# Kernel tuning notes

Hardware: AMD Instinct MI355X
Metric: run time of the kernel (lower is better)

Reference implementation:

```python
import jax, jax.numpy as jnp
import numpy as np

B, S, D, H = 128, 2048, 512, 512


def setup_inputs() -> dict:
    key = jax.random.key(0)
    ks = jax.random.split(key, 8)
    inputs = jax.random.normal(ks[0], (B, D), dtype=jnp.float32)
    contexts = jax.random.normal(ks[1], (B, S, D), dtype=jnp.float32)
    mask = jax.random.randint(ks[2], (B, S), 0, 2).astype(bool)  # True = masked out
    W_in = jax.random.normal(ks[3], (H, D), dtype=jnp.float32) * (1.0 / np.sqrt(D))
    b_in = jnp.zeros((H,), dtype=jnp.float32)
    W_ctx = jax.random.normal(ks[4], (H, D), dtype=jnp.float32) * (1.0 / np.sqrt(D))  # Conv1d k=1 weight
    b_ctx = jnp.zeros((H,), dtype=jnp.float32)
    V = jax.random.normal(ks[5], (H,), dtype=jnp.float32) * (1.0 / np.sqrt(H))
    return {"inputs": inputs, "contexts": contexts, "mask": mask,
            "W_in": W_in, "b_in": b_in, "W_ctx": W_ctx, "b_ctx": b_ctx, "V": V}


def reference(inputs, contexts, mask, W_in, b_in, W_ctx, b_ctx, V):
    # query projection (nn.Linear): [B, H]
    q = inputs @ W_in.T + b_in
    # context projection (Conv1d kernel=1 over permuted [B, D, S]): [B, H, S]
    ctx = jnp.einsum('hd,bsd->bhs', W_ctx, contexts) + b_ctx[None, :, None]
    # additive (Bahdanau) score: V . tanh(q + ctx) over H -> [B, S]
    att = jnp.einsum('h,bhs->bs', V, jnp.tanh(q[:, :, None] + ctx))
    att = jnp.where(mask, -jnp.inf, att)
    score = jax.nn.softmax(att, axis=1)  # nn.Softmax() on 2D -> dim=1 (S)
    # weighted sum of projected contexts: [B, H]
    hidden = jnp.einsum('bhs,bs->bh', ctx, score)
    return hidden, score
```

## Files before the change

kernel.cpp:

```cpp
#include <hip/hip_runtime.h>
#include <hip/hip_bf16.h>
#include <math.h>


#define B_N 128
#define S_N 2048
#define D_N 512
#define H_N 512

typedef __attribute__((ext_vector_type(8))) short bf16x8;
typedef __attribute__((ext_vector_type(4))) float f32x4;

__device__ __forceinline__ unsigned short f2bf(float x) {
  union { float f; unsigned int u; } v; v.f = x;
  unsigned int r = v.u + 0x7fffu + ((v.u >> 16) & 1u);
  return (unsigned short)(r >> 16);
}

__device__ __forceinline__ float tanh_fast(float x) {
  float ax = fabsf(x);
  float e = __expf(2.0f * ax);
  float t = 1.0f - 2.0f / (e + 1.0f);
  return copysignf(t, x);
}

__global__ void detect_mask_kernel(const unsigned int* __restrict__ mask,
                                   int* __restrict__ flag) {
  int tid = threadIdx.x;
  unsigned int bad = 0;
  for (int i = tid; i < 256; i += 64) bad |= (mask[i] > 1u) ? 1u : 0u;
  unsigned long long b = __ballot(bad != 0);
  if (tid == 0) *flag = (b == 0ull) ? 1 : 0;
}

__global__ __launch_bounds__(256) void packw_kernel(const float* __restrict__ Wc,
                                                    unsigned short* __restrict__ wpack) {
  int idx = blockIdx.x * 256 + threadIdx.x;
  int h = idx >> 9;
  int kg = idx & 511;
  int t = kg >> 6, kk = kg & 63;
  int byte = t * 65536 + h * 128 + ((kk * 2) ^ ((h & 7) << 4));
  *(unsigned short*)((char*)wpack + byte) = f2bf(Wc[idx]);
}

__global__ __launch_bounds__(256) void qproj_kernel(const float* __restrict__ inp,
    const float* __restrict__ Win, const float* __restrict__ bin,
    const float* __restrict__ bctx, float* __restrict__ qpb) {
  int b = blockIdx.x, tid = threadIdx.x;
  __shared__ float xin[D_N];
  xin[tid] = inp[b * D_N + tid];
  xin[tid + 256] = inp[b * D_N + tid + 256];
  __syncthreads();
  #pragma unroll
  for (int hh = 0; hh < 2; ++hh) {
    int h = tid + hh * 256;
    const float4* wrow = (const float4*)(Win + (size_t)h * D_N);
    float s = 0.f;
    #pragma unroll 4
    for (int i = 0; i < 128; ++i) {
      float4 w = wrow[i];
      s += w.x * xin[i*4] + w.y * xin[i*4+1] + w.z * xin[i*4+2] + w.w * xin[i*4+3];
    }
    qpb[b * H_N + h] = s + bin[h] + bctx[h];
  }
}

__global__ __launch_bounds__(512, 2) void att_kernel(
    const float* __restrict__ ctxs, const void* __restrict__ mask,
    const int* __restrict__ mflag,
    const unsigned short* __restrict__ wpack, const float* __restrict__ qpb,
    const float* __restrict__ Vp, float* __restrict__ att_out) {
  __shared__ char lds[16384 + 65536];
  char* sA = lds;
  char* sB = lds + 16384;
  float* att_red = (float*)lds;

  const int tid  = threadIdx.x;
  const int wid  = tid >> 6;
  const int lane = tid & 63;
  const int ln15 = lane & 15;
  const int lk   = lane >> 4;
  const int wr   = wid >> 2;
  const int wc   = wid & 3;

  const int bx = blockIdx.x;
  const int b  = bx >> 4;
  const int s0 = (bx & 15) * 128;

  f32x4 acc[4][8];
  #pragma unroll
  for (int mi = 0; mi < 4; ++mi)
    #pragma unroll
    for (int ni = 0; ni < 8; ++ni)
      acc[mi][ni] = (f32x4){0.f, 0.f, 0.f, 0.f};

  const float* actx = ctxs + ((size_t)b * S_N + s0) * D_N;

  for (int t = 0; t < 8; ++t) {
    const int k0 = t * 64;
    __syncthreads();
    #pragma unroll
    for (int i = 0; i < 4; ++i) {
      int p = i * 512 + tid;
      int r = p >> 4;
      int c = (p & 15) * 4;
      float4 v = *(const float4*)(actx + (size_t)r * D_N + k0 + c);
      unsigned int lo = (unsigned)f2bf(v.x) | ((unsigned)f2bf(v.y) << 16);
      unsigned int hi = (unsigned)f2bf(v.z) | ((unsigned)f2bf(v.w) << 16);
      int byte = r * 128 + ((c * 2) ^ ((r & 7) << 4));
      *(uint2*)(sA + byte) = make_uint2(lo, hi);
    }
    {
      const char* wsrc = (const char*)wpack + t * 65536;
      #pragma unroll
      for (int i = 0; i < 8; ++i) {
        int ci = wid * 8 + i;
        const char* g = wsrc + ci * 1024 + lane * 16;
        char* l = sB + ci * 1024 + lane * 16;
        __builtin_amdgcn_global_load_lds(
            (const __attribute__((address_space(1))) unsigned int*)g,
            (__attribute__((address_space(3))) unsigned int*)l, 16, 0, 0);
      }
    }
    __syncthreads();
    #pragma unroll
    for (int kk = 0; kk < 64; kk += 32) {
      const int kb2 = (kk + lk * 8) * 2;
      bf16x8 af[4];
      #pragma unroll
      for (int mi = 0; mi < 4; ++mi) {
        int r = wr * 64 + mi * 16 + ln15;
        af[mi] = *(const bf16x8*)(sA + r * 128 + (kb2 ^ ((r & 7) << 4)));
      }
      #pragma unroll
      for (int ni = 0; ni < 8; ++ni) {
        int h = wc * 128 + ni * 16 + ln15;
        bf16x8 bfr = *(const bf16x8*)(sB + h * 128 + (kb2 ^ ((h & 7) << 4)));
        #pragma unroll
        for (int mi = 0; mi < 4; ++mi)
          acc[mi][ni] = __builtin_amdgcn_mfma_f32_16x16x32_bf16(af[mi], bfr, acc[mi][ni], 0, 0, 0);
      }
    }
  }

  float qv[8], vv[8];
  #pragma unroll
  for (int ni = 0; ni < 8; ++ni) {
    int h = wc * 128 + ni * 16 + ln15;
    qv[ni] = qpb[b * H_N + h];
    vv[ni] = Vp[h];
  }
  float part[4][4];
  #pragma unroll
  for (int mi = 0; mi < 4; ++mi)
    #pragma unroll
    for (int j = 0; j < 4; ++j) {
      float s = 0.f;
      #pragma unroll
      for (int ni = 0; ni < 8; ++ni)
        s += vv[ni] * tanh_fast(qv[ni] + acc[mi][ni][j]);
      part[mi][j] = s;
    }
  #pragma unroll
  for (int mi = 0; mi < 4; ++mi)
    #pragma unroll
    for (int j = 0; j < 4; ++j) {
      float p = part[mi][j];
      p += __shfl_xor(p, 1, 64);
      p += __shfl_xor(p, 2, 64);
      p += __shfl_xor(p, 4, 64);
      p += __shfl_xor(p, 8, 64);
      part[mi][j] = p;
    }
  __syncthreads();
  if (ln15 == 0) {
    #pragma unroll
    for (int mi = 0; mi < 4; ++mi)
      #pragma unroll
      for (int j = 0; j < 4; ++j)
        att_red[wid * 64 + mi * 16 + lk * 4 + j] = part[mi][j];
  }
  __syncthreads();
  if (tid < 128) {
    int s = tid;
    int wrr = s >> 6, sl = s & 63;
    float a = att_red[(wrr * 4 + 0) * 64 + sl] + att_red[(wrr * 4 + 1) * 64 + sl]
            + att_red[(wrr * 4 + 2) * 64 + sl] + att_red[(wrr * 4 + 3) * 64 + sl];
    size_t idx = (size_t)b * S_N + s0 + s;
    int mk = (*mflag) ? ((const int*)mask)[idx]
                      : (int)((const unsigned char*)mask)[idx];
    att_out[idx] = mk ? -INFINITY : a;
  }
}

__global__ __launch_bounds__(256) void softmax_kernel(float* __restrict__ score) {
  int b = blockIdx.x, tid = threadIdx.x;
  float* row = score + (size_t)b * S_N;
  float v[8];
  float m = -INFINITY;
  #pragma unroll
  for (int i = 0; i < 8; ++i) { v[i] = row[tid + i * 256]; m = fmaxf(m, v[i]); }
  #pragma unroll
  for (int d = 1; d < 64; d <<= 1) m = fmaxf(m, __shfl_xor(m, d, 64));
  __shared__ float redm[4], reds[4];
  int w = tid >> 6;
  if ((tid & 63) == 0) redm[w] = m;
  __syncthreads();
  m = fmaxf(fmaxf(redm[0], redm[1]), fmaxf(redm[2], redm[3]));
  float ssum = 0.f;
  #pragma unroll
  for (int i = 0; i < 8; ++i) { float e = __expf(v[i] - m); v[i] = e; ssum += e; }
  #pragma unroll
  for (int d = 1; d < 64; d <<= 1) ssum += __shfl_xor(ssum, d, 64);
  if ((tid & 63) == 0) reds[w] = ssum;
  __syncthreads();
  float inv = 1.0f / (reds[0] + reds[1] + reds[2] + reds[3]);
  #pragma unroll
  for (int i = 0; i < 8; ++i) row[tid + i * 256] = v[i] * inv;
}

__global__ __launch_bounds__(256) void cbar_kernel(const float* __restrict__ ctxs,
    const float* __restrict__ score, float* __restrict__ cbar) {
  int bx = blockIdx.x;
  int b = bx >> 3, ch = bx & 7;
  int tid = threadIdx.x;
  int d = tid * 2;
  float ax = 0.f, ay = 0.f;
  const float* base = ctxs + ((size_t)b * S_N + ch * 256) * D_N + d;
  const float* sc = score + (size_t)b * S_N + ch * 256;
  #pragma unroll 4
  for (int s = 0; s < 256; ++s) {
    float w = sc[s];
    float2 c = *(const float2*)(base + (size_t)s * D_N);
    ax += w * c.x; ay += w * c.y;
  }
  atomicAdd(&cbar[b * D_N + d], ax);
  atomicAdd(&cbar[b * D_N + d + 1], ay);
}

__global__ __launch_bounds__(256) void hidden_kernel(const float* __restrict__ Wc,
    const float* __restrict__ bctx, const float* __restrict__ cbar,
    float* __restrict__ hid) {
  int b = blockIdx.x, tid = threadIdx.x;
  __shared__ float cb[D_N];
  cb[tid] = cbar[b * D_N + tid];
  cb[tid + 256] = cbar[b * D_N + tid + 256];
  __syncthreads();
  #pragma unroll
  for (int hh = 0; hh < 2; ++hh) {
    int h = tid + hh * 256;
    const float4* wrow = (const float4*)(Wc + (size_t)h * D_N);
    float s = 0.f;
    #pragma unroll 4
    for (int i = 0; i < 128; ++i) {
      float4 w = wrow[i];
      s += w.x * cb[i*4] + w.y * cb[i*4+1] + w.z * cb[i*4+2] + w.w * cb[i*4+3];
    }
    hid[b * H_N + h] = s + bctx[h];
  }
}

extern "C" void kernel_launch(void* const* d_in, const int* in_sizes, int n_in,
                              void* d_out, int out_size, void* d_ws, size_t ws_size,
                              hipStream_t stream) {
  const float* inputs = (const float*)d_in[0];
  const float* ctxs   = (const float*)d_in[1];
  const void*  mask   = d_in[2];
  const float* Win    = (const float*)d_in[3];
  const float* bin    = (const float*)d_in[4];
  const float* Wc     = (const float*)d_in[5];
  const float* bctx   = (const float*)d_in[6];
  const float* Vp     = (const float*)d_in[7];

  float* hidden = (float*)d_out;
  float* score  = (float*)d_out + B_N * H_N;

  char* ws = (char*)d_ws;
  unsigned short* wpack = (unsigned short*)ws;
  float* qpb  = (float*)(ws + 512 * 1024);
  float* cbar = (float*)(ws + 768 * 1024);
  int*   mflag = (int*)(ws + 1024 * 1024);

  hipMemsetAsync(cbar, 0, B_N * D_N * sizeof(float), stream);
  detect_mask_kernel<<<1, 64, 0, stream>>>((const unsigned int*)mask, mflag);
  packw_kernel<<<H_N * D_N / 256, 256, 0, stream>>>(Wc, wpack);
  qproj_kernel<<<B_N, 256, 0, stream>>>(inputs, Win, bin, bctx, qpb);
  att_kernel<<<B_N * (S_N / 128), 512, 0, stream>>>(ctxs, mask, mflag, wpack, qpb, Vp, score);
  softmax_kernel<<<B_N, 256, 0, stream>>>(score);
  cbar_kernel<<<B_N * 8, 256, 0, stream>>>(ctxs, score, cbar);
  hidden_kernel<<<B_N, 256, 0, stream>>>(Wc, bctx, cbar, hidden);
}
```

Baseline: 1.031 ms.

## Repack weights, halve K-tile in attention GEMM, transpose weights for coalesced GEMVs

Changes the packed W_ctx layout to MFMA fragment order and shrinks the attention GEMM K-step from 64 to 32, with a padded 80-byte A row stride instead of XOR swizzle. This cuts LDS use and drops the launch-bounds occupancy hint. Adds a transpose kernel so the query and hidden projections read weights coalesced as float4 across h. The cbar reduction now uses more blocks and float4 loads. Bf16 conversion moves to the packed intrinsic. The cost is an extra kernel launch, more loop iterations and barriers in the GEMM, and a possible change in LDS bank conflicts.

Result: no change. 1.038 ms (+0.7%).

```diff
diff --git a/kernel.cpp b/kernel.cpp
--- a/kernel.cpp
+++ b/kernel.cpp
@@ -11,10 +11,10 @@
 typedef __attribute__((ext_vector_type(8))) short bf16x8;
 typedef __attribute__((ext_vector_type(4))) float f32x4;
 
-__device__ __forceinline__ unsigned short f2bf(float x) {
-  union { float f; unsigned int u; } v; v.f = x;
-  unsigned int r = v.u + 0x7fffu + ((v.u >> 16) & 1u);
-  return (unsigned short)(r >> 16);
+__device__ __forceinline__ unsigned pk2bf(float x, float y) {
+  union { __hip_bfloat162 h; unsigned u; } cv;
+  cv.h = __float22bfloat162_rn(make_float2(x, y));
+  return cv.u;
 }
 
 __device__ __forceinline__ float tanh_fast(float x) {
@@ -36,43 +36,77 @@
 __global__ __launch_bounds__(256) void packw_kernel(const float* __restrict__ Wc,
                                                     unsigned short* __restrict__ wpack) {
   int idx = blockIdx.x * 256 + threadIdx.x;
-  int h = idx >> 9;
-  int kg = idx & 511;
-  int t = kg >> 6, kk = kg & 63;
-  int byte = t * 65536 + h * 128 + ((kk * 2) ^ ((h & 7) << 4));
-  *(unsigned short*)((char*)wpack + byte) = f2bf(Wc[idx]);
+  int h = idx >> 6;
+  int t = (idx >> 2) & 15;
+  int c = idx & 3;
+  const float* src = Wc + (size_t)h * D_N + t * 32 + c * 8;
+  float4 v0 = *(const float4*)(src);
+  float4 v1 = *(const float4*)(src + 4);
+  uint4 o;
+  o.x = pk2bf(v0.x, v0.y); o.y = pk2bf(v0.z, v0.w);
+  o.z = pk2bf(v1.x, v1.y); o.w = pk2bf(v1.z, v1.w);
+  int byte = t * 32768 + (h >> 4) * 1024 + c * 256 + (h & 15) * 16;
+  *(uint4*)((char*)wpack + byte) = o;
+}
+
+__global__ __launch_bounds__(256) void transpose_kernel(const float* __restrict__ Win,
+    const float* __restrict__ Wc, float* __restrict__ WinT, float* __restrict__ WcT) {
+  __shared__ float tile[64][65];
+  int bid = blockIdx.x;
+  int m = bid >> 6, tl = bid & 63;
+  int tr = (tl >> 3) * 64, tc = (tl & 7) * 64;
+  const float* in = m ? Wc : Win;
+  float* out = m ? WcT : WinT;
+  int tx = threadIdx.x & 63, ty = threadIdx.x >> 6;
+  #pragma unroll
+  for (int i = 0; i < 64; i += 4)
+    tile[i + ty][tx] = in[(size_t)(tr + i + ty) * D_N + tc + tx];
+  __syncthreads();
+  #pragma unroll
+  for (int i = 0; i < 64; i += 4)
+    out[(size_t)(tc + i + ty) * H_N + tr + tx] = tile[tx][i + ty];
 }
 
 __global__ __launch_bounds__(256) void qproj_kernel(const float* __restrict__ inp,
-    const float* __restrict__ Win, const float* __restrict__ bin,
+    const float* __restrict__ WinT, const float* __restrict__ bin,
     const float* __restrict__ bctx, float* __restrict__ qpb) {
   int b = blockIdx.x, tid = threadIdx.x;
   __shared__ float xin[D_N];
+  __shared__ float4 red[128];
   xin[tid] = inp[b * D_N + tid];
   xin[tid + 256] = inp[b * D_N + tid + 256];
   __syncthreads();
-  #pragma unroll
-  for (int hh = 0; hh < 2; ++hh) {
-    int h = tid + hh * 256;
-    const float4* wrow = (const float4*)(Win + (size_t)h * D_N);
-    float s = 0.f;
-    #pragma unroll 4
-    for (int i = 0; i < 128; ++i) {
-      float4 w = wrow[i];
-      s += w.x * xin[i*4] + w.y * xin[i*4+1] + w.z * xin[i*4+2] + w.w * xin[i*4+3];
-    }
-    qpb[b * H_N + h] = s + bin[h] + bctx[h];
-  }
-}
-
-__global__ __launch_bounds__(512, 2) void att_kernel(
+  int hq = tid & 127;
+  int dp = tid >> 7;
+  const float4* wt = (const float4*)WinT;
+  float4 a = make_float4(0.f, 0.f, 0.f, 0.f);
+  #pragma unroll 8
+  for (int d = dp; d < D_N; d += 2) {
+    float xs = xin[d];
+    float4 w = wt[d * 128 + hq];
+    a.x += xs * w.x; a.y += xs * w.y; a.z += xs * w.z; a.w += xs * w.w;
+  }
+  if (dp == 1) red[hq] = a;
+  __syncthreads();
+  if (dp == 0) {
+    float4 r = red[hq];
+    float4 bi = ((const float4*)bin)[hq];
+    float4 bc = ((const float4*)bctx)[hq];
+    float4 o;
+    o.x = a.x + r.x + bi.x + bc.x; o.y = a.y + r.y + bi.y + bc.y;
+    o.z = a.z + r.z + bi.z + bc.z; o.w = a.w + r.w + bi.w + bc.w;
+    ((float4*)qpb)[b * 128 + hq] = o;
+  }
+}
+
+__global__ __launch_bounds__(512) void att_kernel(
     const float* __restrict__ ctxs, const void* __restrict__ mask,
     const int* __restrict__ mflag,
     const unsigned short* __restrict__ wpack, const float* __restrict__ qpb,
     const float* __restrict__ Vp, float* __restrict__ att_out) {
-  __shared__ char lds[16384 + 65536];
+  __shared__ char lds[10240 + 32768];
   char* sA = lds;
-  char* sB = lds + 16384;
+  char* sB = lds + 10240;
   float* att_red = (float*)lds;
 
   const int tid  = threadIdx.x;
@@ -95,51 +129,44 @@
       acc[mi][ni] = (f32x4){0.f, 0.f, 0.f, 0.f};
 
   const float* actx = ctxs + ((size_t)b * S_N + s0) * D_N;
-
-  for (int t = 0; t < 8; ++t) {
-    const int k0 = t * 64;
+  const int r0  = tid >> 3;
+  const int c40 = tid & 7;
+
+  for (int t = 0; t < 16; ++t) {
+    const int k0 = t * 32;
     __syncthreads();
-    #pragma unroll
-    for (int i = 0; i < 4; ++i) {
-      int p = i * 512 + tid;
-      int r = p >> 4;
-      int c = (p & 15) * 4;
-      float4 v = *(const float4*)(actx + (size_t)r * D_N + k0 + c);
-      unsigned int lo = (unsigned)f2bf(v.x) | ((unsigned)f2bf(v.y) << 16);
-      unsigned int hi = (unsigned)f2bf(v.z) | ((unsigned)f2bf(v.w) << 16);
-      int byte = r * 128 + ((c * 2) ^ ((r & 7) << 4));
-      *(uint2*)(sA + byte) = make_uint2(lo, hi);
-    }
     {
-      const char* wsrc = (const char*)wpack + t * 65536;
+      const float* g0 = actx + (size_t)r0 * D_N + k0 + c40 * 4;
+      float4 v0 = *(const float4*)g0;
+      float4 v1 = *(const float4*)(g0 + (size_t)64 * D_N);
+      *(uint2*)(sA + r0 * 80 + c40 * 8) =
+          make_uint2(pk2bf(v0.x, v0.y), pk2bf(v0.z, v0.w));
+      *(uint2*)(sA + (r0 + 64) * 80 + c40 * 8) =
+          make_uint2(pk2bf(v1.x, v1.y), pk2bf(v1.z, v1.w));
+    }
+    {
+      const char* wsrc = (const char*)wpack + t * 32768 + wid * 4096;
+      char* ldst = sB + wid * 4096;
       #pragma unroll
-      for (int i = 0; i < 8; ++i) {
-        int ci = wid * 8 + i;
-        const char* g = wsrc + ci * 1024 + lane * 16;
-        char* l = sB + ci * 1024 + lane * 16;
+      for (int c = 0; c < 4; ++c)
         __builtin_amdgcn_global_load_lds(
-            (const __attribute__((address_space(1))) unsigned int*)g,
-            (__attribute__((address_space(3))) unsigned int*)l, 16, 0, 0);
-      }
+            (const __attribute__((address_space(1))) unsigned int*)(wsrc + c * 1024 + lane * 16),
+            (__attribute__((address_space(3))) unsigned int*)(ldst + c * 1024 + lane * 16),
+            16, 0, 0);
     }
     __syncthreads();
-    #pragma unroll
-    for (int kk = 0; kk < 64; kk += 32) {
-      const int kb2 = (kk + lk * 8) * 2;
-      bf16x8 af[4];
+    bf16x8 af[4];
+    #pragma unroll
+    for (int mi = 0; mi < 4; ++mi) {
+      int r = wr * 64 + mi * 16 + ln15;
+      af[mi] = *(const bf16x8*)(sA + r * 80 + lk * 16);
+    }
+    #pragma unroll
+    for (int ni = 0; ni < 8; ++ni) {
+      bf16x8 bfr = *(const bf16x8*)(sB + (wc * 8 + ni) * 1024 + lk * 256 + ln15 * 16);
       #pragma unroll
-      for (int mi = 0; mi < 4; ++mi) {
-        int r = wr * 64 + mi * 16 + ln15;
-        af[mi] = *(const bf16x8*)(sA + r * 128 + (kb2 ^ ((r & 7) << 4)));
-      }
-      #pragma unroll
-      for (int ni = 0; ni < 8; ++ni) {
-        int h = wc * 128 + ni * 16 + ln15;
-        bf16x8 bfr = *(const bf16x8*)(sB + h * 128 + (kb2 ^ ((h & 7) << 4)));
-        #pragma unroll
-        for (int mi = 0; mi < 4; ++mi)
-          acc[mi][ni] = __builtin_amdgcn_mfma_f32_16x16x32_bf16(af[mi], bfr, acc[mi][ni], 0, 0, 0);
-      }
+      for (int mi = 0; mi < 4; ++mi)
+        acc[mi][ni] = __builtin_amdgcn_mfma_f32_16x16x32_bf16(af[mi], bfr, acc[mi][ni], 0, 0, 0);
     }
   }
 
@@ -222,41 +249,62 @@
 __global__ __launch_bounds__(256) void cbar_kernel(const float* __restrict__ ctxs,
     const float* __restrict__ score, float* __restrict__ cbar) {
   int bx = blockIdx.x;
-  int b = bx >> 3, ch = bx & 7;
+  int b = bx >> 4, ch = bx & 15;
   int tid = threadIdx.x;
-  int d = tid * 2;
-  float ax = 0.f, ay = 0.f;
-  const float* base = ctxs + ((size_t)b * S_N + ch * 256) * D_N + d;
-  const float* sc = score + (size_t)b * S_N + ch * 256;
+  __shared__ float sc[128];
+  __shared__ float4 red[128];
+  if (tid < 128) sc[tid] = score[(size_t)b * S_N + ch * 128 + tid];
+  __syncthreads();
+  int dq = tid & 127;
+  int sp = tid >> 7;
+  const float4* c4 = (const float4*)(ctxs + ((size_t)b * S_N + ch * 128) * D_N);
+  float4 a = make_float4(0.f, 0.f, 0.f, 0.f);
   #pragma unroll 4
-  for (int s = 0; s < 256; ++s) {
+  for (int s = sp; s < 128; s += 2) {
     float w = sc[s];
-    float2 c = *(const float2*)(base + (size_t)s * D_N);
-    ax += w * c.x; ay += w * c.y;
-  }
-  atomicAdd(&cbar[b * D_N + d], ax);
-  atomicAdd(&cbar[b * D_N + d + 1], ay);
-}
-
-__global__ __launch_bounds__(256) void hidden_kernel(const float* __restrict__ Wc,
+    float4 c = c4[s * 128 + dq];
+    a.x += w * c.x; a.y += w * c.y; a.z += w * c.z; a.w += w * c.w;
+  }
+  if (sp == 1) red[dq] = a;
+  __syncthreads();
+  if (sp == 0) {
+    float4 r = red[dq];
+    float* dst = cbar + b * D_N + dq * 4;
+    atomicAdd(dst + 0, a.x + r.x);
+    atomicAdd(dst + 1, a.y + r.y);
+    atomicAdd(dst + 2, a.z + r.z);
+    atomicAdd(dst + 3, a.w + r.w);
+  }
+}
+
+__global__ __launch_bounds__(256) void hidden_kernel(const float* __restrict__ WcT,
     const float* __restrict__ bctx, const float* __restrict__ cbar,
     float* __restrict__ hid) {
   int b = blockIdx.x, tid = threadIdx.x;
   __shared__ float cb[D_N];
+  __shared__ float4 red[128];
   cb[tid] = cbar[b * D_N + tid];
   cb[tid + 256] = cbar[b * D_N + tid + 256];
   __syncthreads();
-  #pragma unroll
-  for (int hh = 0; hh < 2; ++hh) {
-    int h = tid + hh * 256;
-    const float4* wrow = (const float4*)(Wc + (size_t)h * D_N);
-    float s = 0.f;
-    #pragma unroll 4
-    for (int i = 0; i < 128; ++i) {
-      float4 w = wrow[i];
-      s += w.x * cb[i*4] + w.y * cb[i*4+1] + w.z * cb[i*4+2] + w.w * cb[i*4+3];
-    }
-    hid[b * H_N + h] = s + bctx[h];
+  int hq = tid & 127;
+  int dp = tid >> 7;
+  const float4* wt = (const float4*)WcT;
+  float4 a = make_float4(0.f, 0.f, 0.f, 0.f);
+  #pragma unroll 8
+  for (int d = dp; d < D_N; d += 2) {
+    float xs = cb[d];
+    float4 w = wt[d * 128 + hq];
+    a.x += xs * w.x; a.y += xs * w.y; a.z += xs * w.z; a.w += xs * w.w;
+  }
+  if (dp == 1) red[hq] = a;
+  __syncthreads();
+  if (dp == 0) {
+    float4 r = red[hq];
+    float4 bc = ((const float4*)bctx)[hq];
+    float4 o;
+    o.x = a.x + r.x + bc.x; o.y = a.y + r.y + bc.y;
+    o.z = a.z + r.z + bc.z; o.w = a.w + r.w + bc.w;
+    ((float4*)hid)[b * 128 + hq] = o;
   }
 }
 
@@ -277,16 +325,19 @@
 
   char* ws = (char*)d_ws;
   unsigned short* wpack = (unsigned short*)ws;
-  float* qpb  = (float*)(ws + 512 * 1024);
-  float* cbar = (float*)(ws + 768 * 1024);
-  int*   mflag = (int*)(ws + 1024 * 1024);
+  float* WinT = (float*)(ws + 512 * 1024);
+  float* WcT  = (float*)(ws + 1536 * 1024);
+  float* qpb  = (float*)(ws + 2560 * 1024);
+  float* cbar = (float*)(ws + 2816 * 1024);
+  int*   mflag = (int*)(ws + 3072 * 1024);
 
   hipMemsetAsync(cbar, 0, B_N * D_N * sizeof(float), stream);
   detect_mask_kernel<<<1, 64, 0, stream>>>((const unsigned int*)mask, mflag);
-  packw_kernel<<<H_N * D_N / 256, 256, 0, stream>>>(Wc, wpack);
-  qproj_kernel<<<B_N, 256, 0, stream>>>(inputs, Win, bin, bctx, qpb);
+  packw_kernel<<<128, 256, 0, stream>>>(Wc, wpack);
+  transpose_kernel<<<128, 256, 0, stream>>>(Win, Wc, WinT, WcT);
+  qproj_kernel<<<B_N, 256, 0, stream>>>(inputs, WinT, bin, bctx, qpb);
   att_kernel<<<B_N * (S_N / 128), 512, 0, stream>>>(ctxs, mask, mflag, wpack, qpb, Vp, score);
   softmax_kernel<<<B_N, 256, 0, stream>>>(score);
-  cbar_kernel<<<B_N * 8, 256, 0, stream>>>(ctxs, score, cbar);
-  hidden_kernel<<<B_N, 256, 0, stream>>>(Wc, bctx, cbar, hidden);
-}
+  cbar_kernel<<<B_N * 16, 256, 0, stream>>>(ctxs, score, cbar);
+  hidden_kernel<<<B_N, 256, 0, stream>>>(WcT, bctx, cbar, hidden);
+}
```
